# Kernel optimization log

Measured on AMD Instinct MI355X. Metric: run time of the kernel, lower is better.

## Reference

```python
import jax, jax.numpy as jnp
import numpy as np

N, P, D = 262144, 128, 64
EPS = 1e-5
NEG = -1e30


def setup_inputs() -> dict:
    key = jax.random.key(0)
    ks = jax.random.split(key, 12)
    feature = jax.random.normal(ks[0], (N, D), jnp.float32)
    feature_geo = jax.random.normal(ks[1], (N, D), jnp.float32)
    xyz = jax.random.uniform(ks[2], (N, 3), jnp.float32)
    centers = jax.random.uniform(ks[3], (3,), jnp.float32)
    plane_center = jax.random.uniform(ks[4], (P, 3), jnp.float32)
    nrm = jax.random.normal(ks[5], (P, 3), jnp.float32)
    plane_normal = nrm / jnp.linalg.norm(nrm, axis=1, keepdims=True)
    lo = 0.3 * jax.random.uniform(ks[6], (P, 3), jnp.float32)
    hi = 0.5 + 0.5 * jax.random.uniform(ks[7], (P, 3), jnp.float32)
    # exactly two active axes per plane (one axis of the aabb is zeroed)
    ax = jnp.arange(P) % 3
    keep = (jnp.arange(3)[None, :] != ax[:, None]).astype(jnp.float32)
    plane_xyz_min = lo * keep
    plane_xyz_max = hi * keep
    w1 = 0.05 * jax.random.normal(ks[8], (2 * D, D), jnp.float32)
    b1 = jnp.zeros((D,), jnp.float32)
    w2 = 0.05 * jax.random.normal(ks[9], (D, D), jnp.float32)
    b2 = jnp.zeros((D,), jnp.float32)
    w3 = 0.05 * jax.random.normal(ks[10], (D, 1), jnp.float32)
    b3 = jnp.zeros((1,), jnp.float32)
    g1 = jnp.ones((D,), jnp.float32); be1 = jnp.zeros((D,), jnp.float32)
    m1 = jnp.zeros((D,), jnp.float32); v1 = jnp.ones((D,), jnp.float32)
    g2 = jnp.ones((D,), jnp.float32); be2 = jnp.zeros((D,), jnp.float32)
    m2 = jnp.zeros((D,), jnp.float32); v2 = jnp.ones((D,), jnp.float32)
    return dict(feature=feature, feature_geo=feature_geo, xyz=xyz, centers=centers,
                plane_center=plane_center, plane_normal=plane_normal,
                plane_xyz_min=plane_xyz_min, plane_xyz_max=plane_xyz_max,
                w1=w1, b1=b1, g1=g1, be1=be1, m1=m1, v1=v1,
                w2=w2, b2=b2, g2=g2, be2=be2, m2=m2, v2=v2,
                w3=w3, b3=b3)


def _bn(x, g, b, m, v):
    return (x - m) * (g * jax.lax.rsqrt(v + EPS)) + b


def reference(feature, feature_geo, xyz, centers, plane_center, plane_normal,
              plane_xyz_min, plane_xyz_max, w1, b1, g1, be1, m1, v1,
              w2, b2, g2, be2, m2, v2, w3, b3):
    clouds = xyz + centers                                   # [N,3]
    f = jnp.concatenate([feature, feature_geo], axis=1)      # [N,2D]
    # 1x1 conv MLP == per-point matmul (fc1 -> fc2 with BN+ReLU, fc3)
    h1 = jax.nn.relu(_bn(f @ w1 + b1, g1, be1, m1, v1))      # [N,D]
    h2 = jax.nn.relu(_bn(h1 @ w2 + b2, g2, be2, m2, v2))     # [N,D]
    scores = jax.nn.relu(h2 @ w3 + b3)[:, 0]                 # [N]
    # per-plane aabb mask over the two active axes (xyz_max != 0)
    active = plane_xyz_max != 0                              # [P,3]
    in_rng = (clouds[None] >= plane_xyz_min[:, None]) & (clouds[None] < plane_xyz_max[:, None])
    range_mask = jnp.all(in_rng | ~active[:, None, :], axis=-1)   # [P,N]
    # point-to-plane distance: |(clouds - center) . normal|
    dots = clouds @ plane_normal.T                           # [N,P]
    offs = jnp.sum(plane_center * plane_normal, axis=1)      # [P]
    dist = jnp.abs(dots - offs[None, :]).T                   # [P,N]
    mask = range_mask & (dist < 0.1)                         # [P,N]
    sig = jax.nn.sigmoid(scores)                             # [N]
    on_mask = mask & (sig > 0.5)[None, :]
    off_mask = mask & (sig <= 0.5)[None, :]

    def pool(m):  # masked max-pool of fc2 features over points of one plane
        val = jnp.max(jnp.where(m[:, None], h2, NEG), axis=0)     # [D]
        return jnp.where(jnp.any(m), val, 0.0)

    on_feat = jax.lax.map(pool, on_mask)                     # [P,D]
    off_feat = jax.lax.map(pool, off_mask)                   # [P,D]
    scores_masked = jnp.where(mask, scores[None, :], 0.0)    # [P,N]
    return scores_masked, mask, on_mask, off_mask, on_feat, off_feat
```

## Files before the change

kernel.cpp:

```cpp
#include <hip/hip_runtime.h>
#include <hip/hip_bf16.h>
#include <math.h>

#define NPTS 262144
#define NP   128
#define DD   64
#define NWORDS (NPTS / 64)

__global__ __launch_bounds__(256) void prep_kernel(
    const float* __restrict__ plane_center, const float* __restrict__ plane_normal,
    const float* __restrict__ pmin, const float* __restrict__ pmax,
    float* __restrict__ packed, float* __restrict__ out_feats)
{
    const int t = threadIdx.x;
    out_feats[blockIdx.x * 256 + t] = 0.0f;
    if (blockIdx.x == 0 && t < NP) {
        float n0 = plane_normal[t*3+0], n1 = plane_normal[t*3+1], n2 = plane_normal[t*3+2];
        float c0 = plane_center[t*3+0], c1 = plane_center[t*3+1], c2 = plane_center[t*3+2];
        float off = (c0*n0 + c1*n1) + c2*n2;
        float4* pp = reinterpret_cast<float4*>(packed) + t * 3;
        pp[0] = make_float4(n0, n1, n2, off);
        pp[1] = make_float4(pmin[t*3+0], pmin[t*3+1], pmin[t*3+2], 0.0f);
        pp[2] = make_float4(pmax[t*3+0], pmax[t*3+1], pmax[t*3+2], 0.0f);
    }
}

__global__ __launch_bounds__(256, 4) void fused_kernel(
    const float* __restrict__ feature, const float* __restrict__ feature_geo,
    const float* __restrict__ xyz, const float* __restrict__ centers,
    const float* __restrict__ packed,
    const float* __restrict__ w1, const float* __restrict__ b1,
    const float* __restrict__ g1, const float* __restrict__ be1,
    const float* __restrict__ m1, const float* __restrict__ v1,
    const float* __restrict__ w2, const float* __restrict__ b2,
    const float* __restrict__ g2, const float* __restrict__ be2,
    const float* __restrict__ m2, const float* __restrict__ v2,
    const float* __restrict__ w3, const float* __restrict__ b3,
    float* __restrict__ h2_out,
    float* __restrict__ out_sm, float* __restrict__ out_mask,
    float* __restrict__ out_on, float* __restrict__ out_off,
    unsigned long long* __restrict__ hitOn, unsigned long long* __restrict__ hitOff)
{
    const int t = threadIdx.x;
    const int n = blockIdx.x * 256 + t;

    const float c0 = xyz[n*3+0] + centers[0];
    const float c1 = xyz[n*3+1] + centers[1];
    const float c2 = xyz[n*3+2] + centers[2];

    float acc[DD];
#pragma unroll
    for (int j = 0; j < DD; ++j) acc[j] = 0.0f;

    const float4* fA = reinterpret_cast<const float4*>(feature) + (size_t)n * 16;
    const float4* fB = reinterpret_cast<const float4*>(feature_geo) + (size_t)n * 16;
    float4 nxt = fA[0];
#pragma unroll 1
    for (int q = 0; q < 16; ++q) {
        const float4 fv = nxt;
        nxt = fA[(q + 1) & 15];
        const float* wr = w1 + q * 4 * DD;
#pragma unroll
        for (int j = 0; j < DD; ++j) acc[j] = fmaf(fv.x, wr[j], acc[j]);
#pragma unroll
        for (int j = 0; j < DD; ++j) acc[j] = fmaf(fv.y, wr[DD + j], acc[j]);
#pragma unroll
        for (int j = 0; j < DD; ++j) acc[j] = fmaf(fv.z, wr[2 * DD + j], acc[j]);
#pragma unroll
        for (int j = 0; j < DD; ++j) acc[j] = fmaf(fv.w, wr[3 * DD + j], acc[j]);
    }
    const float* w1b = w1 + DD * DD;
    nxt = fB[0];
#pragma unroll 1
    for (int q = 0; q < 16; ++q) {
        const float4 fv = nxt;
        nxt = fB[(q + 1) & 15];
        const float* wr = w1b + q * 4 * DD;
#pragma unroll
        for (int j = 0; j < DD; ++j) acc[j] = fmaf(fv.x, wr[j], acc[j]);
#pragma unroll
        for (int j = 0; j < DD; ++j) acc[j] = fmaf(fv.y, wr[DD + j], acc[j]);
#pragma unroll
        for (int j = 0; j < DD; ++j) acc[j] = fmaf(fv.z, wr[2 * DD + j], acc[j]);
#pragma unroll
        for (int j = 0; j < DD; ++j) acc[j] = fmaf(fv.w, wr[3 * DD + j], acc[j]);
    }
    float h1[DD];
#pragma unroll
    for (int j = 0; j < DD; ++j) {
        float sc = g1[j] * (1.0f / sqrtf(v1[j] + 1e-5f));
        float h  = fmaf(acc[j] + b1[j] - m1[j], sc, be1[j]);
        h1[j] = fmaxf(h, 0.0f);
    }

    float s = 0.0f;
    float4* o = reinterpret_cast<float4*>(h2_out) + (size_t)n * 16;
#pragma unroll 1
    for (int hh = 0; hh < 2; ++hh) {
        float a2[32];
#pragma unroll
        for (int j = 0; j < 32; ++j) a2[j] = 0.0f;
        const float* w2h = w2 + hh * 32;
#pragma unroll 1
        for (int q = 0; q < 16; ++q) {
            const float fx = h1[4*q+0], fy = h1[4*q+1], fz = h1[4*q+2], fw = h1[4*q+3];
            const float* wr = w2h + q * 4 * DD;
#pragma unroll
            for (int j = 0; j < 32; ++j) a2[j] = fmaf(fx, wr[j], a2[j]);
#pragma unroll
            for (int j = 0; j < 32; ++j) a2[j] = fmaf(fy, wr[DD + j], a2[j]);
#pragma unroll
            for (int j = 0; j < 32; ++j) a2[j] = fmaf(fz, wr[2 * DD + j], a2[j]);
#pragma unroll
            for (int j = 0; j < 32; ++j) a2[j] = fmaf(fw, wr[3 * DD + j], a2[j]);
        }
#pragma unroll
        for (int j = 0; j < 32; ++j) {
            const int jj = hh * 32 + j;
            float sc = g2[jj] * (1.0f / sqrtf(v2[jj] + 1e-5f));
            float h  = fmaf(a2[j] + b2[jj] - m2[jj], sc, be2[jj]);
            h = fmaxf(h, 0.0f);
            a2[j] = h;
            s = fmaf(h, w3[jj], s);
        }
#pragma unroll
        for (int q = 0; q < 8; ++q)
            o[hh * 8 + q] = make_float4(a2[4*q+0], a2[4*q+1], a2[4*q+2], a2[4*q+3]);
    }
    s += b3[0];
    const float score = fmaxf(s, 0.0f);

    const bool on  = (0.5f + 0.5f * tanhf(0.5f * score)) > 0.5f;
    const int lane = t & 63;
    const int word = n >> 6;

    const float4* pp = reinterpret_cast<const float4*>(packed);
    float4 nrm = pp[0], mn = pp[1], mx = pp[2];
#pragma unroll 1
    for (int p = 0; p < NP; ++p) {
        const int pn = ((p + 1) & 127) * 3;
        float4 nrmN = pp[pn + 0];
        float4 mnN  = pp[pn + 1];
        float4 mxN  = pp[pn + 2];
        float d = fabsf(fmaf(c2, nrm.z, fmaf(c1, nrm.y, c0 * nrm.x)) - nrm.w);
        bool ok0 = (mx.x == 0.0f) | ((c0 >= mn.x) & (c0 < mx.x));
        bool ok1 = (mx.y == 0.0f) | ((c1 >= mn.y) & (c1 < mx.y));
        bool ok2 = (mx.z == 0.0f) | ((c2 >= mn.z) & (c2 < mx.z));
        bool mk  = ok0 & ok1 & ok2 & (d < 0.1f);
        size_t idx = (size_t)p * NPTS + n;
        bool mon  = mk & on;
        bool moff = mk & (!on);
        __builtin_nontemporal_store(mk ? score : 0.0f, &out_sm[idx]);
        __builtin_nontemporal_store(mk ? 1.0f : 0.0f,  &out_mask[idx]);
        __builtin_nontemporal_store(mon ? 1.0f : 0.0f, &out_on[idx]);
        __builtin_nontemporal_store(moff ? 1.0f : 0.0f,&out_off[idx]);
        unsigned long long bOn  = __ballot(mon);
        unsigned long long bOff = __ballot(moff);
        if (lane == 0) {
            hitOn [(size_t)p * NWORDS + word] = bOn;
            hitOff[(size_t)p * NWORDS + word] = bOff;
        }
        nrm = nrmN; mn = mnN; mx = mxN;
    }
}

__global__ __launch_bounds__(256) void pool_kernel(
    const float* __restrict__ h2,
    const unsigned long long* __restrict__ hitOn,
    const unsigned long long* __restrict__ hitOff,
    int* __restrict__ out_feats_i)
{
    __shared__ float tile[128 * DD];
    __shared__ unsigned long long bm[2][NP][2];
    const int t = threadIdx.x;
    const int lane = t & 63;
    const int wv = t >> 6;

    float accOn[32], accOff[32];
#pragma unroll
    for (int i = 0; i < 32; ++i) { accOn[i] = 0.0f; accOff[i] = 0.0f; }

    for (int cc = 0; cc < 4; ++cc) {
        const int chunk = blockIdx.x * 4 + cc;
        const int base  = chunk * 128;
        const float4* src = reinterpret_cast<const float4*>(h2 + (size_t)base * DD);
        float4* dst = reinterpret_cast<float4*>(tile);
#pragma unroll
        for (int q = 0; q < 8; ++q) dst[t + q * 256] = src[t + q * 256];
        {
            const int p = t & 127;
            const int half = t >> 7;
            const unsigned long long* hsrc = half ? hitOff : hitOn;
            const int w0 = chunk * 2;
            bm[half][p][0] = hsrc[(size_t)p * NWORDS + w0 + 0];
            bm[half][p][1] = hsrc[(size_t)p * NWORDS + w0 + 1];
        }
        __syncthreads();

#pragma unroll
        for (int i = 0; i < 32; ++i) {
            const int p = wv * 32 + i;
            unsigned long long m;
            m = bm[0][p][0];
            while (m) { int nn = __builtin_ctzll(m); m &= m - 1;
                        accOn[i]  = fmaxf(accOn[i],  tile[nn * DD + lane]); }
            m = bm[0][p][1];
            while (m) { int nn = __builtin_ctzll(m); m &= m - 1;
                        accOn[i]  = fmaxf(accOn[i],  tile[(64 + nn) * DD + lane]); }
            m = bm[1][p][0];
            while (m) { int nn = __builtin_ctzll(m); m &= m - 1;
                        accOff[i] = fmaxf(accOff[i], tile[nn * DD + lane]); }
            m = bm[1][p][1];
            while (m) { int nn = __builtin_ctzll(m); m &= m - 1;
                        accOff[i] = fmaxf(accOff[i], tile[(64 + nn) * DD + lane]); }
        }
        __syncthreads();
    }
#pragma unroll
    for (int i = 0; i < 32; ++i) {
        const int p = wv * 32 + i;
        if (accOn[i]  != 0.0f) atomicMax(&out_feats_i[p * DD + lane],            __float_as_int(accOn[i]));
        if (accOff[i] != 0.0f) atomicMax(&out_feats_i[NP * DD + p * DD + lane],  __float_as_int(accOff[i]));
    }
}

extern "C" void kernel_launch(void* const* d_in, const int* in_sizes, int n_in,
                              void* d_out, int out_size, void* d_ws, size_t ws_size,
                              hipStream_t stream) {
    const float* feature      = (const float*)d_in[0];
    const float* feature_geo  = (const float*)d_in[1];
    const float* xyz          = (const float*)d_in[2];
    const float* centers      = (const float*)d_in[3];
    const float* plane_center = (const float*)d_in[4];
    const float* plane_normal = (const float*)d_in[5];
    const float* pmin         = (const float*)d_in[6];
    const float* pmax         = (const float*)d_in[7];
    const float* w1 = (const float*)d_in[8];
    const float* b1 = (const float*)d_in[9];
    const float* g1 = (const float*)d_in[10];
    const float* be1 = (const float*)d_in[11];
    const float* m1 = (const float*)d_in[12];
    const float* v1 = (const float*)d_in[13];
    const float* w2 = (const float*)d_in[14];
    const float* b2 = (const float*)d_in[15];
    const float* g2 = (const float*)d_in[16];
    const float* be2 = (const float*)d_in[17];
    const float* m2 = (const float*)d_in[18];
    const float* v2 = (const float*)d_in[19];
    const float* w3 = (const float*)d_in[20];
    const float* b3 = (const float*)d_in[21];

    float* out = (float*)d_out;
    const size_t PN = (size_t)NP * NPTS;
    float* out_sm    = out;
    float* out_mask  = out + PN;
    float* out_on    = out + 2 * PN;
    float* out_off   = out + 3 * PN;
    float* out_feats = out + 4 * PN;

    float* h2     = (float*)d_ws;
    unsigned long long* hitOn  = (unsigned long long*)(h2 + (size_t)NPTS * DD);
    unsigned long long* hitOff = hitOn + (size_t)NP * NWORDS;
    float* packed = (float*)(hitOff + (size_t)NP * NWORDS);

    prep_kernel<<<64, 256, 0, stream>>>(
        plane_center, plane_normal, pmin, pmax, packed, out_feats);
    fused_kernel<<<NPTS / 256, 256, 0, stream>>>(
        feature, feature_geo, xyz, centers, packed,
        w1, b1, g1, be1, m1, v1, w2, b2, g2, be2, m2, v2, w3, b3,
        h2, out_sm, out_mask, out_on, out_off, hitOn, hitOff);
    pool_kernel<<<512, 256, 0, stream>>>(h2, hitOn, hitOff, (int*)out_feats);
}
```

Baseline: 851.8 us.

## Interleave plane mask computation and mask stores into the fc1 GEMM loop

Plane membership tests and out_mask stores move inside the first-layer matmul loops, four planes per iteration, so these memory writes overlap with FMA-bound compute. The per-plane bits are kept in two 64-bit registers and reused in the tail loop, which now writes only the score, on and off outputs plus the ballots. The explicit software prefetch of the feature float4 is dropped. This adds register pressure at 4 waves per SIMD and may change how the compiler schedules the FMA chain.

```diff
diff --git a/kernel.cpp b/kernel.cpp
--- a/kernel.cpp
+++ b/kernel.cpp
@@ -43,22 +43,25 @@
 {
     const int t = threadIdx.x;
     const int n = blockIdx.x * 256 + t;
+    const int lane = t & 63;
+    const int word = n >> 6;
 
     const float c0 = xyz[n*3+0] + centers[0];
     const float c1 = xyz[n*3+1] + centers[1];
     const float c2 = xyz[n*3+2] + centers[2];
 
+    const float4* pp = reinterpret_cast<const float4*>(packed);
+    unsigned long long mklo = 0ull, mkhi = 0ull;
+
     float acc[DD];
 #pragma unroll
     for (int j = 0; j < DD; ++j) acc[j] = 0.0f;
 
     const float4* fA = reinterpret_cast<const float4*>(feature) + (size_t)n * 16;
     const float4* fB = reinterpret_cast<const float4*>(feature_geo) + (size_t)n * 16;
-    float4 nxt = fA[0];
 #pragma unroll 1
     for (int q = 0; q < 16; ++q) {
-        const float4 fv = nxt;
-        nxt = fA[(q + 1) & 15];
+        const float4 fv = fA[q];
         const float* wr = w1 + q * 4 * DD;
 #pragma unroll
         for (int j = 0; j < DD; ++j) acc[j] = fmaf(fv.x, wr[j], acc[j]);
@@ -68,13 +71,25 @@
         for (int j = 0; j < DD; ++j) acc[j] = fmaf(fv.z, wr[2 * DD + j], acc[j]);
 #pragma unroll
         for (int j = 0; j < DD; ++j) acc[j] = fmaf(fv.w, wr[3 * DD + j], acc[j]);
+#pragma unroll
+        for (int u = 0; u < 4; ++u) {
+            const int p = q * 4 + u;
+            const float4 nrm = pp[p*3+0];
+            const float4 mn  = pp[p*3+1];
+            const float4 mx  = pp[p*3+2];
+            float d = fabsf(fmaf(c2, nrm.z, fmaf(c1, nrm.y, c0 * nrm.x)) - nrm.w);
+            bool ok0 = (mx.x == 0.0f) | ((c0 >= mn.x) & (c0 < mx.x));
+            bool ok1 = (mx.y == 0.0f) | ((c1 >= mn.y) & (c1 < mx.y));
+            bool ok2 = (mx.z == 0.0f) | ((c2 >= mn.z) & (c2 < mx.z));
+            bool mk  = ok0 & ok1 & ok2 & (d < 0.1f);
+            __builtin_nontemporal_store(mk ? 1.0f : 0.0f, &out_mask[(size_t)p * NPTS + n]);
+            mklo |= ((unsigned long long)mk) << p;
+        }
     }
     const float* w1b = w1 + DD * DD;
-    nxt = fB[0];
 #pragma unroll 1
     for (int q = 0; q < 16; ++q) {
-        const float4 fv = nxt;
-        nxt = fB[(q + 1) & 15];
+        const float4 fv = fB[q];
         const float* wr = w1b + q * 4 * DD;
 #pragma unroll
         for (int j = 0; j < DD; ++j) acc[j] = fmaf(fv.x, wr[j], acc[j]);
@@ -84,6 +99,20 @@
         for (int j = 0; j < DD; ++j) acc[j] = fmaf(fv.z, wr[2 * DD + j], acc[j]);
 #pragma unroll
         for (int j = 0; j < DD; ++j) acc[j] = fmaf(fv.w, wr[3 * DD + j], acc[j]);
+#pragma unroll
+        for (int u = 0; u < 4; ++u) {
+            const int p = 64 + q * 4 + u;
+            const float4 nrm = pp[p*3+0];
+            const float4 mn  = pp[p*3+1];
+            const float4 mx  = pp[p*3+2];
+            float d = fabsf(fmaf(c2, nrm.z, fmaf(c1, nrm.y, c0 * nrm.x)) - nrm.w);
+            bool ok0 = (mx.x == 0.0f) | ((c0 >= mn.x) & (c0 < mx.x));
+            bool ok1 = (mx.y == 0.0f) | ((c1 >= mn.y) & (c1 < mx.y));
+            bool ok2 = (mx.z == 0.0f) | ((c2 >= mn.z) & (c2 < mx.z));
+            bool mk  = ok0 & ok1 & ok2 & (d < 0.1f);
+            __builtin_nontemporal_store(mk ? 1.0f : 0.0f, &out_mask[(size_t)p * NPTS + n]);
+            mkhi |= ((unsigned long long)mk) << (p - 64);
+        }
     }
     float h1[DD];
 #pragma unroll
@@ -130,37 +159,39 @@
     s += b3[0];
     const float score = fmaxf(s, 0.0f);
 
-    const bool on  = (0.5f + 0.5f * tanhf(0.5f * score)) > 0.5f;
-    const int lane = t & 63;
-    const int word = n >> 6;
-
-    const float4* pp = reinterpret_cast<const float4*>(packed);
-    float4 nrm = pp[0], mn = pp[1], mx = pp[2];
-#pragma unroll 1
-    for (int p = 0; p < NP; ++p) {
-        const int pn = ((p + 1) & 127) * 3;
-        float4 nrmN = pp[pn + 0];
-        float4 mnN  = pp[pn + 1];
-        float4 mxN  = pp[pn + 2];
-        float d = fabsf(fmaf(c2, nrm.z, fmaf(c1, nrm.y, c0 * nrm.x)) - nrm.w);
-        bool ok0 = (mx.x == 0.0f) | ((c0 >= mn.x) & (c0 < mx.x));
-        bool ok1 = (mx.y == 0.0f) | ((c1 >= mn.y) & (c1 < mx.y));
-        bool ok2 = (mx.z == 0.0f) | ((c2 >= mn.z) & (c2 < mx.z));
-        bool mk  = ok0 & ok1 & ok2 & (d < 0.1f);
-        size_t idx = (size_t)p * NPTS + n;
-        bool mon  = mk & on;
-        bool moff = mk & (!on);
+    const bool on = (0.5f + 0.5f * tanhf(0.5f * score)) > 0.5f;
+
+#pragma unroll 1
+    for (int p = 0; p < 64; ++p) {
+        const bool mk = (mklo >> p) & 1ull;
+        const size_t idx = (size_t)p * NPTS + n;
+        const bool mon  = mk & on;
+        const bool moff = mk & (!on);
         __builtin_nontemporal_store(mk ? score : 0.0f, &out_sm[idx]);
-        __builtin_nontemporal_store(mk ? 1.0f : 0.0f,  &out_mask[idx]);
         __builtin_nontemporal_store(mon ? 1.0f : 0.0f, &out_on[idx]);
-        __builtin_nontemporal_store(moff ? 1.0f : 0.0f,&out_off[idx]);
+        __builtin_nontemporal_store(moff ? 1.0f : 0.0f, &out_off[idx]);
         unsigned long long bOn  = __ballot(mon);
         unsigned long long bOff = __ballot(moff);
         if (lane == 0) {
             hitOn [(size_t)p * NWORDS + word] = bOn;
             hitOff[(size_t)p * NWORDS + word] = bOff;
         }
-        nrm = nrmN; mn = mnN; mx = mxN;
+    }
+#pragma unroll 1
+    for (int p = 64; p < 128; ++p) {
+        const bool mk = (mkhi >> (p - 64)) & 1ull;
+        const size_t idx = (size_t)p * NPTS + n;
+        const bool mon  = mk & on;
+        const bool moff = mk & (!on);
+        __builtin_nontemporal_store(mk ? score : 0.0f, &out_sm[idx]);
+        __builtin_nontemporal_store(mon ? 1.0f : 0.0f, &out_on[idx]);
+        __builtin_nontemporal_store(moff ? 1.0f : 0.0f, &out_off[idx]);
+        unsigned long long bOn  = __ballot(mon);
+        unsigned long long bOff = __ballot(moff);
+        if (lane == 0) {
+            hitOn [(size_t)p * NWORDS + word] = bOn;
+            hitOff[(size_t)p * NWORDS + word] = bOff;
+        }
     }
 }
 
```

New measurement: 876.8 us. 1.03x slower.
